# Kernel optimization log

Measured on AMD Instinct MI355X. Metric: run time of the kernel, lower is better.

The kernel has to match this reference:

```python
import jax, jax.numpy as jnp
import numpy as np

N = 20000
E = 320000
IN_DIM = 128
HID = 64
HEADS = 8
OUT_DIM = 128
NEG_SLOPE = 0.2  # PyG GATConv default leaky_relu slope


def _glorot(key, shape):
    fan_in = shape[0] if len(shape) > 1 else shape[-1]
    return jax.random.normal(key, shape, dtype=jnp.float32) / jnp.sqrt(jnp.float32(fan_in))


def setup_inputs() -> dict:
    key = jax.random.key(0)
    ks = jax.random.split(key, 16)
    x = jax.random.normal(ks[0], (N, IN_DIM), dtype=jnp.float32)
    edge_index = jax.random.randint(ks[1], (2, E), 0, N, dtype=jnp.int32)
    HC = HEADS * HID
    return {
        "x": x,
        "edge_index": edge_index,
        # layer 1: in -> heads*hid (concat)
        "W1": _glorot(ks[2], (IN_DIM, HC)),
        "a_src1": _glorot(ks[3], (HEADS, HID)),
        "a_dst1": _glorot(ks[4], (HEADS, HID)),
        "b1": jnp.zeros((HC,), jnp.float32),
        # layer 2: heads*hid -> heads*hid (concat)
        "W2": _glorot(ks[5], (HC, HC)),
        "a_src2": _glorot(ks[6], (HEADS, HID)),
        "a_dst2": _glorot(ks[7], (HEADS, HID)),
        "b2": jnp.zeros((HC,), jnp.float32),
        # layer 3: heads*hid -> out, heads=1, concat=False
        "W3": _glorot(ks[8], (HC, OUT_DIM)),
        "a_src3": _glorot(ks[9], (1, OUT_DIM)),
        "a_dst3": _glorot(ks[10], (1, OUT_DIM)),
        "b3": jnp.zeros((OUT_DIM,), jnp.float32),
    }


def _gat_layer(x, src, dst, W, a_src, a_dst, b, heads, concat):
    # x: [N, F_in] -> h: [N, H, C]
    n = x.shape[0]
    h = (x @ W).reshape(n, heads, -1)
    # per-node attention half-logits: [N, H]
    al_src = jnp.sum(h * a_src[None], axis=-1)
    al_dst = jnp.sum(h * a_dst[None], axis=-1)
    # per-edge logits with leaky relu: [E, H]
    e = jax.nn.leaky_relu(al_src[src] + al_dst[dst], NEG_SLOPE)
    # segment softmax over incoming edges of each dst node
    emax = jax.ops.segment_max(e, dst, num_segments=n)
    ex = jnp.exp(e - emax[dst])
    den = jax.ops.segment_sum(ex, dst, num_segments=n)
    alpha = ex / (den[dst] + 1e-16)
    # weighted scatter-aggregate of source features: [E, H, C] -> [N, H, C]
    out = jax.ops.segment_sum(h[src] * alpha[:, :, None], dst, num_segments=n)
    out = out.reshape(n, -1) if concat else out.mean(axis=1)
    return out + b


def reference(x, edge_index, W1, a_src1, a_dst1, b1, W2, a_src2, a_dst2, b2,
              W3, a_src3, a_dst3, b3):
    # PyG GATConv adds self-loops by default
    loops = jnp.arange(N, dtype=edge_index.dtype)
    src = jnp.concatenate([edge_index[0], loops])
    dst = jnp.concatenate([edge_index[1], loops])
    # eval mode: dropout is identity
    h = _gat_layer(x, src, dst, W1, a_src1, a_dst1, b1, HEADS, True)
    h = jax.nn.elu(h)
    h = _gat_layer(h, src, dst, W2, a_src2, a_dst2, b2, HEADS, True)
    h = jax.nn.elu(h)
    out = _gat_layer(h, src, dst, W3, a_src3, a_dst3, b3, 1, False)
    return out
```

## Files before the change

### kernel.cpp

```cpp
#include <hip/hip_runtime.h>
#include <math.h>

#define NN 20000
#define EE 320000
#define ETOT 340000
#define NHEADS 8
#define HID 64
#define HCV 512
#define IND 128
#define OUTD 128
#define NEG_SLOPE 0.2f
#define LOG2E 1.4426950408889634f

typedef __attribute__((ext_vector_type(8))) _Float16 half8;
typedef __attribute__((ext_vector_type(4))) _Float16 half4;
typedef __attribute__((ext_vector_type(4))) float floatx4;

#define S1 (IND * HCV)
#define S2 (HCV * HCV)
#define S3 (HCV * OUTD)
#define XTOT (NN * IND)

#define NT1 64
#define NT2 320
#define NT_TOT 384
#define XB 2500
__global__ __launch_bounds__(256) void prep_kernel(const float* __restrict__ W1,
                                                   const float* __restrict__ W2,
                                                   const float* __restrict__ W3,
                                                   const float* __restrict__ x,
                                                   _Float16* __restrict__ T1,
                                                   _Float16* __restrict__ T2,
                                                   _Float16* __restrict__ T3,
                                                   _Float16* __restrict__ xh,
                                                   int* __restrict__ cnt) {
    int b = blockIdx.x;
    int tid = threadIdx.x;
    if (b < NT_TOT) {
        __shared__ _Float16 tile[32][34];
        const float* W; _Float16* T; int K, N, tb;
        if (b < NT1)      { W = W1; T = T1; K = IND; N = HCV;  tb = b; }
        else if (b < NT2) { W = W2; T = T2; K = HCV; N = HCV;  tb = b - NT1; }
        else              { W = W3; T = T3; K = HCV; N = OUTD; tb = b - NT2; }
        int ntn = N >> 5;
        int k0 = (tb / ntn) * 32, n0 = (tb % ntn) * 32;
        int tx = tid & 31, ty0 = tid >> 5;
        #pragma unroll
        for (int i = 0; i < 4; i++) {
            int ty = ty0 + 8 * i;
            tile[ty][tx] = (_Float16)W[(size_t)(k0 + ty) * N + n0 + tx];
        }
        __syncthreads();
        #pragma unroll
        for (int i = 0; i < 4; i++) {
            int ty = ty0 + 8 * i;
            T[(size_t)(n0 + ty) * K + k0 + tx] = tile[tx][ty];
        }
    } else if (b < NT_TOT + XB) {
        int idx = (b - NT_TOT) * 256 + tid;
        int j = idx * 4;
        float4 v = *(const float4*)&x[j];
        half4 o;
        o[0] = (_Float16)v.x; o[1] = (_Float16)v.y;
        o[2] = (_Float16)v.z; o[3] = (_Float16)v.w;
        *(half4*)&xh[j] = o;
    } else {
        int idx = (b - NT_TOT - XB) * 256 + tid;
        if (idx < NN) cnt[idx] = 0;
    }
}


__global__ void count_kernel(const int* __restrict__ ei, int* __restrict__ cnt) {
    int i = blockIdx.x * blockDim.x + threadIdx.x;
    if (i >= ETOT) return;
    int v = (i < EE) ? ei[EE + i] : (i - EE);
    atomicAdd(&cnt[v], 1);
}

#define SCH 20
__global__ __launch_bounds__(1024) void scan_kernel(const int* __restrict__ cnt,
                                                    int* __restrict__ row_ptr,
                                                    int* __restrict__ cursor) {
    __shared__ int wtot[16];
    __shared__ int woff[16];
    int t = threadIdx.x;
    int lane = t & 63;
    int wid = t >> 6;
    int base = t * SCH;
    int vals[SCH];
    int s = 0;
    #pragma unroll
    for (int i = 0; i < SCH; i++) {
        int idx = base + i;
        int v = (idx < NN) ? cnt[idx] : 0;
        vals[i] = v;
        s += v;
    }
    int incl = s;
    #pragma unroll
    for (int off = 1; off < 64; off <<= 1) {
        int u = __shfl_up(incl, off);
        if (lane >= off) incl += u;
    }
    int excl = incl - s;
    if (lane == 63) wtot[wid] = incl;
    __syncthreads();
    if (t == 0) {
        int run = 0;
        #pragma unroll
        for (int j = 0; j < 16; j++) { woff[j] = run; run += wtot[j]; }
        row_ptr[NN] = run;
    }
    __syncthreads();
    int run = woff[wid] + excl;
    #pragma unroll
    for (int i = 0; i < SCH; i++) {
        int idx = base + i;
        if (idx < NN) { row_ptr[idx] = run; cursor[idx] = run; run += vals[i]; }
    }
}

__global__ void fill_kernel(const int* __restrict__ ei, int* __restrict__ cursor,
                            int* __restrict__ csr_src) {
    int i = blockIdx.x * blockDim.x + threadIdx.x;
    if (i >= ETOT) return;
    int u, v;
    if (i < EE) { u = ei[i]; v = ei[EE + i]; }
    else        { u = i - EE; v = i - EE; }
    int pos = atomicAdd(&cursor[v], 1);
    csr_src[pos] = u;
}

#define BK 32
__global__ __launch_bounds__(512) void gemm_al(const _Float16* __restrict__ A,
                                               const _Float16* __restrict__ Bt,
                                               _Float16* __restrict__ C16,
                                               const float* __restrict__ a_src,
                                               const float* __restrict__ a_dst,
                                               float* __restrict__ als2,
                                               float* __restrict__ ald2,
                                               int M, int K) {
    __shared__ _Float16 sA[128 * BK];
    __shared__ _Float16 sB[128 * BK];
    __shared__ float psum_s[4][128];
    __shared__ float psum_d[4][128];
    int tid = threadIdx.x;
    int lane = tid & 63;
    int wid = tid >> 6;
    int wv_m = wid >> 2;
    int wv_n = wid & 3;
    int m0 = blockIdx.x * 128, n0 = blockIdx.y * 128;
    int quad = lane >> 4;
    int l15 = lane & 15;

    int phys = wid * 1024 + lane * 16;
    int logical = phys ^ (((phys >> 7) & 3) << 4);
    int lrow = logical >> 6;
    int lcol = (logical >> 4) & 3;
    int gmA = m0 + lrow;
    const _Float16* gA = A + (size_t)gmA * K + lcol * 8;
    const _Float16* gB = Bt + (size_t)(n0 + lrow) * K + lcol * 8;
    bool aok = (gmA < M);
    _Float16* lA = sA + wid * 512;
    _Float16* lB = sB + wid * 512;

    int ra[4], rb[2];
    #pragma unroll
    for (int i = 0; i < 4; i++) {
        int lb = (wv_m * 64 + i * 16 + l15) * 64 + quad * 16;
        ra[i] = lb ^ (((lb >> 7) & 3) << 4);
    }
    #pragma unroll
    for (int j = 0; j < 2; j++) {
        int lb = (wv_n * 32 + j * 16 + l15) * 64 + quad * 16;
        rb[j] = lb ^ (((lb >> 7) & 3) << 4);
    }

    floatx4 acc[4][2] = {};

    for (int k0 = 0; k0 < K; k0 += BK) {
        if (aok)
            __builtin_amdgcn_global_load_lds(
                (const __attribute__((address_space(1))) void*)(gA + k0),
                (__attribute__((address_space(3))) void*)lA, 16, 0, 0);
        __builtin_amdgcn_global_load_lds(
            (const __attribute__((address_space(1))) void*)(gB + k0),
            (__attribute__((address_space(3))) void*)lB, 16, 0, 0);
        __syncthreads();
        half8 a[4], b[2];
        #pragma unroll
        for (int i = 0; i < 4; i++)
            a[i] = *(const half8*)((const char*)sA + ra[i]);
        #pragma unroll
        for (int j = 0; j < 2; j++)
            b[j] = *(const half8*)((const char*)sB + rb[j]);
        #pragma unroll
        for (int i = 0; i < 4; i++)
            #pragma unroll
            for (int j = 0; j < 2; j++)
                acc[i][j] = __builtin_amdgcn_mfma_f32_16x16x32_f16(a[i], b[j], acc[i][j], 0, 0, 0);
        __syncthreads();
    }
    #pragma unroll
    for (int i = 0; i < 4; i++) {
        #pragma unroll
        for (int r = 0; r < 4; r++) {
            int gm = m0 + wv_m * 64 + i * 16 + quad * 4 + r;
            if (gm < M) {
                #pragma unroll
                for (int j = 0; j < 2; j++)
                    C16[(size_t)gm * HCV + n0 + wv_n * 32 + j * 16 + l15] = (_Float16)acc[i][j][r];
            }
        }
    }
    int h0 = n0 >> 6;
    int hh = h0 + (wv_n >> 1);
    float as_v[2], ad_v[2];
    #pragma unroll
    for (int j = 0; j < 2; j++) {
        int dim = (wv_n * 32 + j * 16 + l15) & 63;
        as_v[j] = a_src[hh * HID + dim] * LOG2E;
        ad_v[j] = a_dst[hh * HID + dim] * LOG2E;
    }
    #pragma unroll
    for (int i = 0; i < 4; i++) {
        #pragma unroll
        for (int r = 0; r < 4; r++) {
            float ps = acc[i][0][r] * as_v[0] + acc[i][1][r] * as_v[1];
            float pd = acc[i][0][r] * ad_v[0] + acc[i][1][r] * ad_v[1];
            #pragma unroll
            for (int off = 1; off <= 8; off <<= 1) {
                ps += __shfl_xor(ps, off);
                pd += __shfl_xor(pd, off);
            }
            if (l15 == 0) {
                int row = wv_m * 64 + i * 16 + quad * 4 + r;
                psum_s[wv_n][row] = ps;
                psum_d[wv_n][row] = pd;
            }
        }
    }
    __syncthreads();
    if (tid < 128) {
        int gm = m0 + tid;
        if (gm < M) {
            als2[(size_t)h0 * NN + gm]       = psum_s[0][tid] + psum_s[1][tid];
            als2[(size_t)(h0 + 1) * NN + gm] = psum_s[2][tid] + psum_s[3][tid];
            ald2[(size_t)h0 * NN + gm]       = psum_d[0][tid] + psum_d[1][tid];
            ald2[(size_t)(h0 + 1) * NN + gm] = psum_d[2][tid] + psum_d[3][tid];
        }
    }
}

__global__ __launch_bounds__(512) void gemm3(const _Float16* __restrict__ A,
                                             const _Float16* __restrict__ Bt,
                                             _Float16* __restrict__ C16,
                                             const float* __restrict__ a_src,
                                             const float* __restrict__ a_dst,
                                             float* __restrict__ als,
                                             float* __restrict__ ald,
                                             int M, int K) {
    __shared__ _Float16 sA[128 * BK];
    __shared__ _Float16 sB[128 * BK];
    __shared__ float psum_s[4][128];
    __shared__ float psum_d[4][128];
    int tid = threadIdx.x;
    int lane = tid & 63;
    int wid = tid >> 6;
    int wv_m = wid >> 2;
    int wv_n = wid & 3;
    int m0 = blockIdx.x * 128;
    int quad = lane >> 4;
    int l15 = lane & 15;

    int phys = wid * 1024 + lane * 16;
    int logical = phys ^ (((phys >> 7) & 3) << 4);
    int lrow = logical >> 6;
    int lcol = (logical >> 4) & 3;
    int gmA = m0 + lrow;
    const _Float16* gA = A + (size_t)gmA * K + lcol * 8;
    const _Float16* gB = Bt + (size_t)lrow * K + lcol * 8;
    bool aok = (gmA < M);
    _Float16* lA = sA + wid * 512;
    _Float16* lB = sB + wid * 512;

    int ra[4], rb[2];
    #pragma unroll
    for (int i = 0; i < 4; i++) {
        int lb = (wv_m * 64 + i * 16 + l15) * 64 + quad * 16;
        ra[i] = lb ^ (((lb >> 7) & 3) << 4);
    }
    #pragma unroll
    for (int j = 0; j < 2; j++) {
        int lb = (wv_n * 32 + j * 16 + l15) * 64 + quad * 16;
        rb[j] = lb ^ (((lb >> 7) & 3) << 4);
    }

    floatx4 acc[4][2] = {};

    for (int k0 = 0; k0 < K; k0 += BK) {
        if (aok)
            __builtin_amdgcn_global_load_lds(
                (const __attribute__((address_space(1))) void*)(gA + k0),
                (__attribute__((address_space(3))) void*)lA, 16, 0, 0);
        __builtin_amdgcn_global_load_lds(
            (const __attribute__((address_space(1))) void*)(gB + k0),
            (__attribute__((address_space(3))) void*)lB, 16, 0, 0);
        __syncthreads();
        half8 a[4], b[2];
        #pragma unroll
        for (int i = 0; i < 4; i++)
            a[i] = *(const half8*)((const char*)sA + ra[i]);
        #pragma unroll
        for (int j = 0; j < 2; j++)
            b[j] = *(const half8*)((const char*)sB + rb[j]);
        #pragma unroll
        for (int i = 0; i < 4; i++)
            #pragma unroll
            for (int j = 0; j < 2; j++)
                acc[i][j] = __builtin_amdgcn_mfma_f32_16x16x32_f16(a[i], b[j], acc[i][j], 0, 0, 0);
        __syncthreads();
    }
    #pragma unroll
    for (int i = 0; i < 4; i++) {
        #pragma unroll
        for (int r = 0; r < 4; r++) {
            int gm = m0 + wv_m * 64 + i * 16 + quad * 4 + r;
            if (gm < M) {
                #pragma unroll
                for (int j = 0; j < 2; j++)
                    C16[(size_t)gm * OUTD + wv_n * 32 + j * 16 + l15] = (_Float16)acc[i][j][r];
            }
        }
    }
    float as_v[2], ad_v[2];
    #pragma unroll
    for (int j = 0; j < 2; j++) {
        int dim = wv_n * 32 + j * 16 + l15;
        as_v[j] = a_src[dim] * LOG2E;
        ad_v[j] = a_dst[dim] * LOG2E;
    }
    #pragma unroll
    for (int i = 0; i < 4; i++) {
        #pragma unroll
        for (int r = 0; r < 4; r++) {
            float ps = acc[i][0][r] * as_v[0] + acc[i][1][r] * as_v[1];
            float pd = acc[i][0][r] * ad_v[0] + acc[i][1][r] * ad_v[1];
            #pragma unroll
            for (int off = 1; off <= 8; off <<= 1) {
                ps += __shfl_xor(ps, off);
                pd += __shfl_xor(pd, off);
            }
            if (l15 == 0) {
                int row = wv_m * 64 + i * 16 + quad * 4 + r;
                psum_s[wv_n][row] = ps;
                psum_d[wv_n][row] = pd;
            }
        }
    }
    __syncthreads();
    if (tid < 128) {
        int gm = m0 + tid;
        if (gm < M) {
            als[gm] = psum_s[0][tid] + psum_s[1][tid] + psum_s[2][tid] + psum_s[3][tid];
            ald[gm] = psum_d[0][tid] + psum_d[1][tid] + psum_d[2][tid] + psum_d[3][tid];
        }
    }
}

__global__ __launch_bounds__(256) void gather_kernel(const _Float16* __restrict__ h,
                                                     const int* __restrict__ row_ptr,
                                                     const int* __restrict__ csr_src,
                                                     const float* __restrict__ als2,
                                                     const float* __restrict__ ald2,
                                                     const float* __restrict__ bias,
                                                     _Float16* __restrict__ gout) {
    int tid = threadIdx.x;
    int lane = tid & 63;
    int wid = tid >> 6;
    int bid = blockIdx.x;
    int hd = bid & 7;
    int dl = lane & 7;
    int es = (lane >> 3) & 1;
    int sub = lane >> 4;
    int v = (bid >> 3) * 16 + wid * 4 + sub;
    if (v >= NN) return;
    const float* asl = als2 + (size_t)hd * NN;
    float adst = ald2[(size_t)hd * NN + v];
    int s0 = row_ptr[v], s1 = row_ptr[v + 1];
    int mid = (s0 + s1 + 1) >> 1;
    int jb = es ? mid : s0;
    int je = es ? s1 : mid;
    const _Float16* hh = h + hd * HID + dl * 8;
    float acc[8] = {};
    float l = 0.f;
    int j = jb;
    for (; j + 4 <= je; j += 4) {
        int u[4]; float p[4]; half8 xv[4];
        #pragma unroll
        for (int e = 0; e < 4; e++) u[e] = csr_src[j + e];
        #pragma unroll
        for (int e = 0; e < 4; e++) xv[e] = *(const half8*)&hh[(size_t)u[e] * HCV];
        #pragma unroll
        for (int e = 0; e < 4; e++) {
            float t = asl[u[e]] + adst;
            t = fmaxf(t, NEG_SLOPE * t);
            p[e] = exp2f(fminf(t, 115.f));
        }
        #pragma unroll
        for (int e = 0; e < 4; e++) {
            l += p[e];
            #pragma unroll
            for (int k = 0; k < 8; k++)
                acc[k] = fmaf(p[e], (float)xv[e][k], acc[k]);
        }
    }
    for (; j < je; j++) {
        int u0 = csr_src[j];
        half8 x0 = *(const half8*)&hh[(size_t)u0 * HCV];
        float t0 = asl[u0] + adst;
        t0 = fmaxf(t0, NEG_SLOPE * t0);
        float p0 = exp2f(fminf(t0, 115.f));
        l += p0;
        #pragma unroll
        for (int k = 0; k < 8; k++)
            acc[k] = fmaf(p0, (float)x0[k], acc[k]);
    }
    l += __shfl_xor(l, 8);
    #pragma unroll
    for (int k = 0; k < 8; k++)
        acc[k] += __shfl_xor(acc[k], 8);
    if (es == 0) {
        float inv = 1.f / (l + 1e-16f);
        half8 hv;
        #pragma unroll
        for (int k = 0; k < 8; k++) {
            float o = fmaf(acc[k], inv, bias[hd * HID + dl * 8 + k]);
            o = (o > 0.f) ? o : (__expf(o) - 1.f);
            hv[k] = (_Float16)o;
        }
        half8* dst = (half8*)&gout[(size_t)v * HCV + hd * HID + dl * 8];
        __builtin_nontemporal_store(hv, dst);
    }
}

__global__ __launch_bounds__(256) void gather3_kernel(const _Float16* __restrict__ h,
                                                      const int* __restrict__ row_ptr,
                                                      const int* __restrict__ csr_src,
                                                      const float* __restrict__ als,
                                                      const float* __restrict__ ald,
                                                      const float* __restrict__ bias,
                                                      float* __restrict__ out) {
    int tid = threadIdx.x;
    int lane = tid & 63;
    int wid = tid >> 6;
    int bid = blockIdx.x;
    int dh = bid & 1;
    int dl = lane & 7;
    int es = (lane >> 3) & 1;
    int sub = lane >> 4;
    int l16 = lane & 15;
    int v = (bid >> 1) * 16 + wid * 4 + sub;
    if (v >= NN) return;
    float adst = ald[v];
    int s0 = row_ptr[v], s1 = row_ptr[v + 1];
    float m = -INFINITY;
    for (int j = s0 + l16; j < s1; j += 16) {
        int u = csr_src[j];
        float t = als[u] + adst;
        t = fmaxf(t, NEG_SLOPE * t);
        m = fmaxf(m, t);
    }
    #pragma unroll
    for (int off = 1; off <= 8; off <<= 1)
        m = fmaxf(m, __shfl_xor(m, off));
    int mid = (s0 + s1 + 1) >> 1;
    int jb = es ? mid : s0;
    int je = es ? s1 : mid;
    const _Float16* hh = h + dh * 64 + dl * 8;
    float acc[8] = {};
    float l = 0.f;
    int j = jb;
    for (; j + 2 <= je; j += 2) {
        int u0 = csr_src[j], u1 = csr_src[j + 1];
        float t0 = als[u0] + adst;
        float t1 = als[u1] + adst;
        t0 = fmaxf(t0, NEG_SLOPE * t0);
        t1 = fmaxf(t1, NEG_SLOPE * t1);
        float p0 = exp2f(t0 - m);
        float p1 = exp2f(t1 - m);
        half8 x0 = *(const half8*)&hh[(size_t)u0 * OUTD];
        half8 x1 = *(const half8*)&hh[(size_t)u1 * OUTD];
        l += p0 + p1;
        #pragma unroll
        for (int k = 0; k < 8; k++) {
            acc[k] = fmaf(p0, (float)x0[k], acc[k]);
            acc[k] = fmaf(p1, (float)x1[k], acc[k]);
        }
    }
    if (j < je) {
        int u0 = csr_src[j];
        float t0 = als[u0] + adst;
        t0 = fmaxf(t0, NEG_SLOPE * t0);
        float p0 = exp2f(t0 - m);
        half8 x0 = *(const half8*)&hh[(size_t)u0 * OUTD];
        l += p0;
        #pragma unroll
        for (int k = 0; k < 8; k++)
            acc[k] = fmaf(p0, (float)x0[k], acc[k]);
    }
    l += __shfl_xor(l, 8);
    #pragma unroll
    for (int k = 0; k < 8; k++)
        acc[k] += __shfl_xor(acc[k], 8);
    if (es == 0) {
        float inv = 1.f / (l + 1e-16f);
        float4 o0, o1;
        o0.x = fmaf(acc[0], inv, bias[dh * 64 + dl * 8 + 0]);
        o0.y = fmaf(acc[1], inv, bias[dh * 64 + dl * 8 + 1]);
        o0.z = fmaf(acc[2], inv, bias[dh * 64 + dl * 8 + 2]);
        o0.w = fmaf(acc[3], inv, bias[dh * 64 + dl * 8 + 3]);
        o1.x = fmaf(acc[4], inv, bias[dh * 64 + dl * 8 + 4]);
        o1.y = fmaf(acc[5], inv, bias[dh * 64 + dl * 8 + 5]);
        o1.z = fmaf(acc[6], inv, bias[dh * 64 + dl * 8 + 6]);
        o1.w = fmaf(acc[7], inv, bias[dh * 64 + dl * 8 + 7]);
        size_t base = (size_t)v * OUTD + dh * 64 + dl * 8;
        *(float4*)&out[base] = o0;
        *(float4*)&out[base + 4] = o1;
    }
}


extern "C" void kernel_launch(void* const* d_in, const int* in_sizes, int n_in,
                              void* d_out, int out_size, void* d_ws, size_t ws_size,
                              hipStream_t stream) {
    const float* x     = (const float*)d_in[0];
    const int*   ei    = (const int*)d_in[1];
    const float* W1    = (const float*)d_in[2];
    const float* as1   = (const float*)d_in[3];
    const float* ad1   = (const float*)d_in[4];
    const float* b1    = (const float*)d_in[5];
    const float* W2    = (const float*)d_in[6];
    const float* as2   = (const float*)d_in[7];
    const float* ad2   = (const float*)d_in[8];
    const float* b2    = (const float*)d_in[9];
    const float* W3    = (const float*)d_in[10];
    const float* as3   = (const float*)d_in[11];
    const float* ad3   = (const float*)d_in[12];
    const float* b3    = (const float*)d_in[13];
    float* out = (float*)d_out;

    size_t off = 0;
    auto carve = [&](size_t bytes) {
        void* p = (char*)d_ws + off;
        off += (bytes + 255) & ~(size_t)255;
        return p;
    };
    int* row_ptr   = (int*)carve((NN + 1) * sizeof(int));
    int* cursor    = (int*)carve(NN * sizeof(int));
    int* csr_src   = (int*)carve(ETOT * sizeof(int));
    _Float16* xh   = (_Float16*)carve((size_t)NN * IND * sizeof(_Float16));
    _Float16* h1   = (_Float16*)carve((size_t)NN * HCV * sizeof(_Float16));
    _Float16* gact = (_Float16*)carve((size_t)NN * HCV * sizeof(_Float16));
    _Float16* hf16 = (_Float16*)carve((size_t)NN * HCV * sizeof(_Float16));
    _Float16* h3   = (_Float16*)carve((size_t)NN * OUTD * sizeof(_Float16));
    float* als     = (float*)carve((size_t)NN * NHEADS * sizeof(float));
    float* ald     = (float*)carve((size_t)NN * NHEADS * sizeof(float));
    _Float16* W1T  = (_Float16*)carve((size_t)S1 * sizeof(_Float16));
    _Float16* W2T  = (_Float16*)carve((size_t)S2 * sizeof(_Float16));
    _Float16* W3T  = (_Float16*)carve((size_t)S3 * sizeof(_Float16));
    _Float16* gact2 = h1;
    (void)ws_size; (void)n_in; (void)in_sizes; (void)out_size;

    dim3 blk(256);

    int prep_blocks = NT_TOT + XB + (NN + 255) / 256;
    prep_kernel<<<prep_blocks, blk, 0, stream>>>(W1, W2, W3, x, W1T, W2T, W3T, xh, cursor);

    count_kernel<<<(ETOT + 255) / 256, blk, 0, stream>>>(ei, cursor);
    scan_kernel<<<1, 1024, 0, stream>>>(cursor, row_ptr, cursor);
    fill_kernel<<<(ETOT + 255) / 256, blk, 0, stream>>>(ei, cursor, csr_src);

    int mt128 = (NN + 127) / 128;
    int nb4 = (NN + 15) / 16;

    gemm_al<<<dim3(mt128, HCV / 128), dim3(512), 0, stream>>>(xh, W1T, h1, as1, ad1, als, ald, NN, IND);
    gather_kernel<<<dim3(nb4 * 8), blk, 0, stream>>>(h1, row_ptr, csr_src, als, ald, b1, gact);

    gemm_al<<<dim3(mt128, HCV / 128), dim3(512), 0, stream>>>(gact, W2T, hf16, as2, ad2, als, ald, NN, HCV);
    gather_kernel<<<dim3(nb4 * 8), blk, 0, stream>>>(hf16, row_ptr, csr_src, als, ald, b2, gact2);

    gemm3<<<dim3(mt128, 1), dim3(512), 0, stream>>>(gact2, W3T, h3, as3, ad3, als, ald, NN, HCV);
    gather3_kernel<<<dim3(nb4 * 2), blk, 0, stream>>>(h3, row_ptr, csr_src, als, ald, b3, out);
}
```

Before: 310.8 us.

## Double-buffer GEMM LDS tiles and drop max pass in layer-3 gather softmax

The two GEMM kernels now double-buffer their A/B shared-memory tiles, so the next K-slice's global-to-LDS load is issued before the current slice's MFMAs and one barrier per iteration goes away. The layer-3 gather kernel drops its separate pass that computed the per-node max logit. It uses exp2 directly with the logit clamped at 115 to avoid overflow, and unrolls the edge loop by four so more feature loads are in flight. Skipping max subtraction risks accuracy if logits get large, and double buffering doubles the LDS footprint, which may lower occupancy.

```diff
diff --git a/kernel.cpp b/kernel.cpp
--- a/kernel.cpp
+++ b/kernel.cpp
@@ -133,6 +133,8 @@
 }
 
 #define BK 32
+#define TILE_E (128 * BK)
+#define TILE_B (TILE_E * 2)
 __global__ __launch_bounds__(512) void gemm_al(const _Float16* __restrict__ A,
                                                const _Float16* __restrict__ Bt,
                                                _Float16* __restrict__ C16,
@@ -141,8 +143,8 @@
                                                float* __restrict__ als2,
                                                float* __restrict__ ald2,
                                                int M, int K) {
-    __shared__ _Float16 sA[128 * BK];
-    __shared__ _Float16 sB[128 * BK];
+    __shared__ _Float16 sA[2 * TILE_E];
+    __shared__ _Float16 sB[2 * TILE_E];
     __shared__ float psum_s[4][128];
     __shared__ float psum_d[4][128];
     int tid = threadIdx.x;
@@ -162,8 +164,6 @@
     const _Float16* gA = A + (size_t)gmA * K + lcol * 8;
     const _Float16* gB = Bt + (size_t)(n0 + lrow) * K + lcol * 8;
     bool aok = (gmA < M);
-    _Float16* lA = sA + wid * 512;
-    _Float16* lB = sB + wid * 512;
 
     int ra[4], rb[2];
     #pragma unroll
@@ -179,28 +179,49 @@
 
     floatx4 acc[4][2] = {};
 
-    for (int k0 = 0; k0 < K; k0 += BK) {
+    int nt = K / BK;
+    int cur = 0;
+    {
+        _Float16* lA = sA + wid * 512;
+        _Float16* lB = sB + wid * 512;
         if (aok)
             __builtin_amdgcn_global_load_lds(
-                (const __attribute__((address_space(1))) void*)(gA + k0),
+                (const __attribute__((address_space(1))) void*)gA,
                 (__attribute__((address_space(3))) void*)lA, 16, 0, 0);
         __builtin_amdgcn_global_load_lds(
-            (const __attribute__((address_space(1))) void*)(gB + k0),
+            (const __attribute__((address_space(1))) void*)gB,
             (__attribute__((address_space(3))) void*)lB, 16, 0, 0);
-        __syncthreads();
+    }
+    __syncthreads();
+    for (int t = 0; t < nt; ++t) {
+        if (t + 1 < nt) {
+            int k1 = (t + 1) * BK;
+            _Float16* lA = sA + (cur ^ 1) * TILE_E + wid * 512;
+            _Float16* lB = sB + (cur ^ 1) * TILE_E + wid * 512;
+            if (aok)
+                __builtin_amdgcn_global_load_lds(
+                    (const __attribute__((address_space(1))) void*)(gA + k1),
+                    (__attribute__((address_space(3))) void*)lA, 16, 0, 0);
+            __builtin_amdgcn_global_load_lds(
+                (const __attribute__((address_space(1))) void*)(gB + k1),
+                (__attribute__((address_space(3))) void*)lB, 16, 0, 0);
+        }
+        const char* bA = (const char*)sA + cur * TILE_B;
+        const char* bB = (const char*)sB + cur * TILE_B;
         half8 a[4], b[2];
         #pragma unroll
         for (int i = 0; i < 4; i++)
-            a[i] = *(const half8*)((const char*)sA + ra[i]);
+            a[i] = *(const half8*)(bA + ra[i]);
         #pragma unroll
         for (int j = 0; j < 2; j++)
-            b[j] = *(const half8*)((const char*)sB + rb[j]);
+            b[j] = *(const half8*)(bB + rb[j]);
         #pragma unroll
         for (int i = 0; i < 4; i++)
             #pragma unroll
             for (int j = 0; j < 2; j++)
                 acc[i][j] = __builtin_amdgcn_mfma_f32_16x16x32_f16(a[i], b[j], acc[i][j], 0, 0, 0);
         __syncthreads();
+        cur ^= 1;
     }
     #pragma unroll
     for (int i = 0; i < 4; i++) {
@@ -261,8 +282,8 @@
                                              float* __restrict__ als,
                                              float* __restrict__ ald,
                                              int M, int K) {
-    __shared__ _Float16 sA[128 * BK];
-    __shared__ _Float16 sB[128 * BK];
+    __shared__ _Float16 sA[2 * TILE_E];
+    __shared__ _Float16 sB[2 * TILE_E];
     __shared__ float psum_s[4][128];
     __shared__ float psum_d[4][128];
     int tid = threadIdx.x;
@@ -282,8 +303,6 @@
     const _Float16* gA = A + (size_t)gmA * K + lcol * 8;
     const _Float16* gB = Bt + (size_t)lrow * K + lcol * 8;
     bool aok = (gmA < M);
-    _Float16* lA = sA + wid * 512;
-    _Float16* lB = sB + wid * 512;
 
     int ra[4], rb[2];
     #pragma unroll
@@ -299,28 +318,49 @@
 
     floatx4 acc[4][2] = {};
 
-    for (int k0 = 0; k0 < K; k0 += BK) {
+    int nt = K / BK;
+    int cur = 0;
+    {
+        _Float16* lA = sA + wid * 512;
+        _Float16* lB = sB + wid * 512;
         if (aok)
             __builtin_amdgcn_global_load_lds(
-                (const __attribute__((address_space(1))) void*)(gA + k0),
+                (const __attribute__((address_space(1))) void*)gA,
                 (__attribute__((address_space(3))) void*)lA, 16, 0, 0);
         __builtin_amdgcn_global_load_lds(
-            (const __attribute__((address_space(1))) void*)(gB + k0),
+            (const __attribute__((address_space(1))) void*)gB,
             (__attribute__((address_space(3))) void*)lB, 16, 0, 0);
-        __syncthreads();
+    }
+    __syncthreads();
+    for (int t = 0; t < nt; ++t) {
+        if (t + 1 < nt) {
+            int k1 = (t + 1) * BK;
+            _Float16* lA = sA + (cur ^ 1) * TILE_E + wid * 512;
+            _Float16* lB = sB + (cur ^ 1) * TILE_E + wid * 512;
+            if (aok)
+                __builtin_amdgcn_global_load_lds(
+                    (const __attribute__((address_space(1))) void*)(gA + k1),
+                    (__attribute__((address_space(3))) void*)lA, 16, 0, 0);
+            __builtin_amdgcn_global_load_lds(
+                (const __attribute__((address_space(1))) void*)(gB + k1),
+                (__attribute__((address_space(3))) void*)lB, 16, 0, 0);
+        }
+        const char* bA = (const char*)sA + cur * TILE_B;
+        const char* bB = (const char*)sB + cur * TILE_B;
         half8 a[4], b[2];
         #pragma unroll
         for (int i = 0; i < 4; i++)
-            a[i] = *(const half8*)((const char*)sA + ra[i]);
+            a[i] = *(const half8*)(bA + ra[i]);
         #pragma unroll
         for (int j = 0; j < 2; j++)
-            b[j] = *(const half8*)((const char*)sB + rb[j]);
+            b[j] = *(const half8*)(bB + rb[j]);
         #pragma unroll
         for (int i = 0; i < 4; i++)
             #pragma unroll
             for (int j = 0; j < 2; j++)
                 acc[i][j] = __builtin_amdgcn_mfma_f32_16x16x32_f16(a[i], b[j], acc[i][j], 0, 0, 0);
         __syncthreads();
+        cur ^= 1;
     }
     #pragma unroll
     for (int i = 0; i < 4; i++) {
@@ -460,21 +500,10 @@
     int dl = lane & 7;
     int es = (lane >> 3) & 1;
     int sub = lane >> 4;
-    int l16 = lane & 15;
     int v = (bid >> 1) * 16 + wid * 4 + sub;
     if (v >= NN) return;
     float adst = ald[v];
     int s0 = row_ptr[v], s1 = row_ptr[v + 1];
-    float m = -INFINITY;
-    for (int j = s0 + l16; j < s1; j += 16) {
-        int u = csr_src[j];
-        float t = als[u] + adst;
-        t = fmaxf(t, NEG_SLOPE * t);
-        m = fmaxf(m, t);
-    }
-    #pragma unroll
-    for (int off = 1; off <= 8; off <<= 1)
-        m = fmaxf(m, __shfl_xor(m, off));
     int mid = (s0 + s1 + 1) >> 1;
     int jb = es ? mid : s0;
     int je = es ? s1 : mid;
@@ -482,29 +511,32 @@
     float acc[8] = {};
     float l = 0.f;
     int j = jb;
-    for (; j + 2 <= je; j += 2) {
-        int u0 = csr_src[j], u1 = csr_src[j + 1];
-        float t0 = als[u0] + adst;
-        float t1 = als[u1] + adst;
-        t0 = fmaxf(t0, NEG_SLOPE * t0);
-        t1 = fmaxf(t1, NEG_SLOPE * t1);
-        float p0 = exp2f(t0 - m);
-        float p1 = exp2f(t1 - m);
+    for (; j + 4 <= je; j += 4) {
+        int u[4]; float p[4]; half8 xv[4];
+        #pragma unroll
+        for (int e = 0; e < 4; e++) u[e] = csr_src[j + e];
+        #pragma unroll
+        for (int e = 0; e < 4; e++) xv[e] = *(const half8*)&hh[(size_t)u[e] * OUTD];
+        #pragma unroll
+        for (int e = 0; e < 4; e++) {
+            float t = als[u[e]] + adst;
+            t = fmaxf(t, NEG_SLOPE * t);
+            p[e] = exp2f(fminf(t, 115.f));
+        }
+        #pragma unroll
+        for (int e = 0; e < 4; e++) {
+            l += p[e];
+            #pragma unroll
+            for (int k = 0; k < 8; k++)
+                acc[k] = fmaf(p[e], (float)xv[e][k], acc[k]);
+        }
+    }
+    for (; j < je; j++) {
+        int u0 = csr_src[j];
         half8 x0 = *(const half8*)&hh[(size_t)u0 * OUTD];
-        half8 x1 = *(const half8*)&hh[(size_t)u1 * OUTD];
-        l += p0 + p1;
-        #pragma unroll
-        for (int k = 0; k < 8; k++) {
-            acc[k] = fmaf(p0, (float)x0[k], acc[k]);
-            acc[k] = fmaf(p1, (float)x1[k], acc[k]);
-        }
-    }
-    if (j < je) {
-        int u0 = csr_src[j];
         float t0 = als[u0] + adst;
         t0 = fmaxf(t0, NEG_SLOPE * t0);
-        float p0 = exp2f(t0 - m);
-        half8 x0 = *(const half8*)&hh[(size_t)u0 * OUTD];
+        float p0 = exp2f(fminf(t0, 115.f));
         l += p0;
         #pragma unroll
         for (int k = 0; k < 8; k++)
```

New measurement: 308.4 us. Within noise of the previous version (-0.8%).
